# Kernel tuning notes

Hardware: AMD Instinct MI355X
Metric: run time of the kernel (lower is better)

## Reference

```python
import jax, jax.numpy as jnp
import numpy as np

N = 512          # octave output grid resolution per cube side
M = 256          # input octave resolution
FACTOR = 0.5     # 2 ** (-factor), factor = 1
EPS = 1e-12


def make_cube_faces(n):
    # two triangles per quad on each of the 6 n x n side grids
    idx = np.arange(n * n).reshape(n, n)
    a = idx[:-1, :-1].ravel(); b = idx[:-1, 1:].ravel()
    c = idx[1:, :-1].ravel(); d = idx[1:, 1:].ravel()
    tris = np.concatenate([np.stack([a, b, c], 1), np.stack([b, d, c], 1)], 0)
    faces = np.concatenate([tris + s * n * n for s in range(6)], 0)
    return jnp.asarray(faces, jnp.int32)  # [F, 3]


def to_stacked(t):
    # [1, 6*m*m, 3] -> [6, 3, m, m]
    m = int(round((t.shape[1] // 6) ** 0.5))
    return t.reshape(6, m, m, 3).transpose(0, 3, 1, 2)


def to_vertices(s):
    # [6, 3, m, m] -> [1, 6*m*m, 3]
    return s.transpose(0, 2, 3, 1).reshape(1, -1, 3)


def resize_bilinear_ac(t, n):
    # bilinear, align_corners=True, square input [.., m, m] -> [.., n, n]
    m = t.shape[-1]
    coords = jnp.linspace(0.0, m - 1.0, n)
    i0 = jnp.clip(jnp.floor(coords).astype(jnp.int32), 0, m - 1)
    i1 = jnp.minimum(i0 + 1, m - 1)
    w = (coords - i0).astype(t.dtype)
    t = t[..., i0, :] * (1.0 - w)[:, None] + t[..., i1, :] * w[:, None]
    t = t[..., :, i0] * (1.0 - w) + t[..., :, i1] * w
    return t


def compute_face_normals(vert, faces):
    v = vert[0]                                  # [V, 3]
    v0, v1, v2 = v[faces[:, 0]], v[faces[:, 1]], v[faces[:, 2]]
    fn = jnp.cross(v1 - v0, v2 - v0)             # [F, 3]
    nrm = jnp.linalg.norm(fn, axis=-1, keepdims=True)
    return fn / jnp.maximum(nrm, EPS)


def compute_vertex_normals(vert, faces, face_normals):
    V = vert.shape[1]
    flat_idx = faces.reshape(-1)                          # [3F] f0v0,f0v1,f0v2,...
    rep = jnp.repeat(face_normals, 3, axis=0)             # [3F, 3]
    acc = jax.ops.segment_sum(rep, flat_idx, num_segments=V)  # scatter-add
    nrm = jnp.linalg.norm(acc, axis=-1, keepdims=True)
    return (acc / jnp.maximum(nrm, EPS))[None]            # [1, V, 3]


def get_vertex_normals(vert, faces):
    fn = compute_face_normals(vert, faces)
    normals = compute_vertex_normals(vert, faces, fn)
    stacked = to_stacked(normals)                         # [6, 3, n, n]
    sign = jnp.array([-1.0, 1.0, 1.0, -1.0, -1.0, 1.0], stacked.dtype)
    stacked = stacked * sign[:, None, None, None]
    return to_vertices(stacked)


def setup_inputs() -> dict:
    key = jax.random.key(0)
    k1, k2 = jax.random.split(key)
    vrt = jax.random.normal(k1, (1, 6 * M * M, 3), jnp.float32)
    nrm = jax.random.normal(k2, (1, 6 * M * M, 3), jnp.float32)
    ps = jnp.zeros((6, 1, N, N), jnp.float32)   # nn.Parameter(zeros * noise)
    faces = make_cube_faces(N)
    return {"vrt": vrt, "nrm": nrm, "ps": ps, "faces": faces}


def reference(vrt, nrm, ps, faces):
    vrt_s = resize_bilinear_ac(to_stacked(vrt), N)                 # [6,3,n,n]
    nrm_mag = jnp.linalg.norm(resize_bilinear_ac(to_stacked(nrm), N),
                              axis=1, keepdims=True)               # [6,1,n,n]
    stacked = vrt_s + FACTOR * jax.nn.sigmoid(ps) * nrm_mag
    vert = to_vertices(stacked)                                    # [1, V, 3]
    normals = get_vertex_normals(vert, faces)
    return vert, faces, normals
```

## Files before the change

kernel.cpp:

```cpp
#include <hip/hip_runtime.h>
#include <math.h>

#define NSZ 512
#define MSZ 256
#define NPIX (6 * NSZ * NSZ)
#define NQ   ((NSZ - 1) * (NSZ - 1))
#define NFACE (6 * 2 * NQ)
#define F3TOT (NFACE * 3)
#define TS 32
#define HS (TS + 2)
#define PS 20
#define NVB (6 * 16 * 16)
#define NFT12 (F3TOT / 12)
#define GRID (NVB * 3)

__device__ inline float fast_rcp(float x) {
    float r = __builtin_amdgcn_rcpf(x);
    return r * (2.0f - x * r);
}
__device__ inline float fast_rsqrt(float d) {
    float r = __builtin_amdgcn_rsqf(d);
    return r * (1.5f - 0.5f * d * r * r);
}
__device__ inline float fast_sigmoid(float x) {
    float e = __builtin_amdgcn_exp2f(-1.442695040888963f * x);
    return fast_rcp(1.0f + e);
}

__device__ inline void tri_acc4(const float4 A, const float4 B, const float4 C,
                                float& ax, float& ay, float& az) {
    float e1x = B.x - A.x, e1y = B.y - A.y, e1z = B.z - A.z;
    float e2x = C.x - A.x, e2y = C.y - A.y, e2z = C.z - A.z;
    float nx = e1y * e2z - e1z * e2y;
    float ny = e1z * e2x - e1x * e2z;
    float nz = e1x * e2y - e1y * e2x;
    float d  = fmaxf(nx * nx + ny * ny + nz * nz, 1e-24f);
    float r  = fast_rsqrt(d);
    ax += nx * r; ay += ny * r; az += nz * r;
}

__global__ __launch_bounds__(256) void k_all(const float* __restrict__ vrt,
                                             const float* __restrict__ nrm,
                                             const float* __restrict__ ps,
                                             float* __restrict__ out0,
                                             float* __restrict__ out1,
                                             float* __restrict__ out2) {
    __shared__ float4 spv[PS * PS];
    __shared__ float4 spn[PS * PS];
    __shared__ float4 sv4[HS * HS];

    int blk    = blockIdx.x;
    int triple = blk / 3;
    int pos    = blk - triple * 3;

    if (pos != 0) {
        int t = (triple * 2 + (pos - 1)) * 256 + threadIdx.x;
        if (t >= NFT12) return;
        unsigned ti = 4u * (unsigned)t;
        unsigned s  = ti / (2u * NQ);
        unsigned r1 = ti - s * (2u * NQ);
        unsigned ty = (r1 >= (unsigned)NQ) ? 1u : 0u;
        unsigned qi = r1 - ty * (unsigned)NQ;
        unsigned R  = qi / (NSZ - 1);
        unsigned Q  = qi - R * (NSZ - 1);
        unsigned sbase = s << 18;
        float v[12];
#pragma unroll
        for (int k = 0; k < 4; ++k) {
            unsigned a = sbase + (R << 9) + Q;
            v[3 * k + 0] = (float)(a + (ty ? 1u : 0u));
            v[3 * k + 1] = (float)(a + (ty ? (unsigned)(NSZ + 1) : 1u));
            v[3 * k + 2] = (float)(a + (unsigned)NSZ);
            Q++;
            if (Q == (unsigned)(NSZ - 1)) {
                Q = 0u; R++;
                if (R == (unsigned)(NSZ - 1)) {
                    R = 0u; ty++;
                    if (ty == 2u) { ty = 0u; sbase += (unsigned)(NSZ * NSZ); }
                }
            }
        }
        float4* o = (float4*)out1 + 3 * t;
        o[0] = make_float4(v[0], v[1], v[2],  v[3]);
        o[1] = make_float4(v[4], v[5], v[6],  v[7]);
        o[2] = make_float4(v[8], v[9], v[10], v[11]);
        return;
    }

    int f   = triple >> 8;
    int tl  = triple & 255;
    int tr  = (tl >> 4) * TS;
    int tq  = (tl & 15) * TS;
    int fbm = f * (MSZ * MSZ);
    int fbn = f * (NSZ * NSZ);

    int iy_base = max(0, ((tr - 1) * (MSZ - 1)) / (NSZ - 1));
    int ix_base = max(0, ((tq - 1) * (MSZ - 1)) / (NSZ - 1));

    for (int p = threadIdx.x; p < PS * PS; p += 256) {
        int r = p / PS, c = p - r * PS;
        int iy = min(iy_base + r, MSZ - 1);
        int ix = min(ix_base + c, MSZ - 1);
        int g  = (fbm + iy * MSZ + ix) * 3;
        spv[p] = make_float4(vrt[g], vrt[g + 1], vrt[g + 2], 0.0f);
        spn[p] = make_float4(nrm[g], nrm[g + 1], nrm[g + 2], 0.0f);
    }
    __syncthreads();

    const float scale = 255.0f / 511.0f;
    for (int p = threadIdx.x; p < HS * HS; p += 256) {
        int pr = p / HS, pq = p - pr * HS;
        int y = tr + pr - 1, x = tq + pq - 1;
        int yc = min(max(y, 0), NSZ - 1);
        int xc = min(max(x, 0), NSZ - 1);

        float cy = (float)yc * scale;
        float cx = (float)xc * scale;
        int iy0 = (int)floorf(cy); iy0 = iy0 < 0 ? 0 : (iy0 > MSZ - 1 ? MSZ - 1 : iy0);
        int ix0 = (int)floorf(cx); ix0 = ix0 < 0 ? 0 : (ix0 > MSZ - 1 ? MSZ - 1 : ix0);
        int iy1 = min(iy0 + 1, MSZ - 1);
        int ix1 = min(ix0 + 1, MSZ - 1);
        float wy = cy - (float)iy0;
        float wx = cx - (float)ix0;
        float w00 = (1.0f - wy) * (1.0f - wx);
        float w01 = (1.0f - wy) * wx;
        float w10 = wy * (1.0f - wx);
        float w11 = wy * wx;

        int l00 = (iy0 - iy_base) * PS + (ix0 - ix_base);
        int l01 = (iy0 - iy_base) * PS + (ix1 - ix_base);
        int l10 = (iy1 - iy_base) * PS + (ix0 - ix_base);
        int l11 = (iy1 - iy_base) * PS + (ix1 - ix_base);

        float4 a00 = spv[l00], a01 = spv[l01], a10 = spv[l10], a11 = spv[l11];
        float4 b00 = spn[l00], b01 = spn[l01], b10 = spn[l10], b11 = spn[l11];

        float vx = a00.x * w00 + a01.x * w01 + a10.x * w10 + a11.x * w11;
        float vy = a00.y * w00 + a01.y * w01 + a10.y * w10 + a11.y * w11;
        float vz = a00.z * w00 + a01.z * w01 + a10.z * w10 + a11.z * w11;
        float nx = b00.x * w00 + b01.x * w01 + b10.x * w10 + b11.x * w11;
        float ny = b00.y * w00 + b01.y * w01 + b10.y * w10 + b11.y * w11;
        float nz = b00.z * w00 + b01.z * w01 + b10.z * w10 + b11.z * w11;

        float mag = __builtin_amdgcn_sqrtf(nx * nx + ny * ny + nz * nz);
        float sig = fast_sigmoid(ps[fbn + yc * NSZ + xc]);
        float add = 0.5f * sig * mag;
        float ox = vx + add, oy = vy + add, oz = vz + add;

        sv4[p] = make_float4(ox, oy, oz, 0.0f);
        if (pr >= 1 && pr <= TS && pq >= 1 && pq <= TS) {
            int gi = (fbn + y * NSZ + x) * 3;
            out0[gi + 0] = ox;
            out0[gi + 1] = oy;
            out0[gi + 2] = oz;
        }
    }
    __syncthreads();

    float sg = (f == 1 || f == 2 || f == 5) ? 1.0f : -1.0f;
    for (int p = threadIdx.x; p < TS * TS; p += 256) {
        int r = p >> 5, q = p & 31;
        int lc = (r + 1) * HS + (q + 1);
        float4 C  = sv4[lc];
        float4 W  = sv4[lc - 1];
        float4 E  = sv4[lc + 1];
        float4 Nn = sv4[lc - HS];
        float4 S  = sv4[lc + HS];
        float4 NE = sv4[lc - HS + 1];
        float4 SW = sv4[lc + HS - 1];

        float ax = 0.0f, ay = 0.0f, az = 0.0f;
        tri_acc4(C,  E,  S,  ax, ay, az);
        tri_acc4(W,  C,  SW, ax, ay, az);
        tri_acc4(Nn, NE, C,  ax, ay, az);
        tri_acc4(C,  S,  SW, ax, ay, az);
        tri_acc4(Nn, C,  W,  ax, ay, az);
        tri_acc4(NE, E,  C,  ax, ay, az);

        float d  = fmaxf(ax * ax + ay * ay + az * az, 1e-24f);
        float rs = fast_rsqrt(d) * sg;
        int gi = (fbn + (tr + r) * NSZ + (tq + q)) * 3;
        out2[gi + 0] = ax * rs;
        out2[gi + 1] = ay * rs;
        out2[gi + 2] = az * rs;
    }
}

extern "C" void kernel_launch(void* const* d_in, const int* in_sizes, int n_in,
                              void* d_out, int out_size, void* d_ws, size_t ws_size,
                              hipStream_t stream) {
    const float* vrt = (const float*)d_in[0];
    const float* nrm = (const float*)d_in[1];
    const float* ps  = (const float*)d_in[2];

    float* out0 = (float*)d_out;
    float* out1 = out0 + (size_t)NPIX * 3;
    float* out2 = out1 + (size_t)NFACE * 3;

    k_all<<<GRID, 256, 0, stream>>>(vrt, nrm, ps, out0, out1, out2);
}
```

Before: 32.27 us.

## Compute each triangle normal once per tile in shared memory, then gather per vertex

Replaces the per-vertex recomputation of six adjacent triangle normals with a separate pass that computes the two triangle normals per quad once into shared memory, masking quads that fall outside the mesh. A second pass sums the six incident normals per vertex. The tile is also stored as packed float triples instead of float4, and the shared-memory staging buffers are aliased. This removes about threefold redundant cross products and rsqrt calls, at the cost of an extra barrier pass and strided 3-float LDS accesses that may cause bank conflicts.

```diff
diff --git a/kernel.cpp b/kernel.cpp
--- a/kernel.cpp
+++ b/kernel.cpp
@@ -9,10 +9,12 @@
 #define F3TOT (NFACE * 3)
 #define TS 32
 #define HS (TS + 2)
+#define QS (TS + 1)
 #define PS 20
 #define NVB (6 * 16 * 16)
 #define NFT12 (F3TOT / 12)
 #define GRID (NVB * 3)
+#define USZ (2 * QS * QS * 3)
 
 __device__ inline float fast_rcp(float x) {
     float r = __builtin_amdgcn_rcpf(x);
@@ -25,18 +27,6 @@
 __device__ inline float fast_sigmoid(float x) {
     float e = __builtin_amdgcn_exp2f(-1.442695040888963f * x);
     return fast_rcp(1.0f + e);
-}
-
-__device__ inline void tri_acc4(const float4 A, const float4 B, const float4 C,
-                                float& ax, float& ay, float& az) {
-    float e1x = B.x - A.x, e1y = B.y - A.y, e1z = B.z - A.z;
-    float e2x = C.x - A.x, e2y = C.y - A.y, e2z = C.z - A.z;
-    float nx = e1y * e2z - e1z * e2y;
-    float ny = e1z * e2x - e1x * e2z;
-    float nz = e1x * e2y - e1y * e2x;
-    float d  = fmaxf(nx * nx + ny * ny + nz * nz, 1e-24f);
-    float r  = fast_rsqrt(d);
-    ax += nx * r; ay += ny * r; az += nz * r;
 }
 
 __global__ __launch_bounds__(256) void k_all(const float* __restrict__ vrt,
@@ -45,9 +35,12 @@
                                              float* __restrict__ out0,
                                              float* __restrict__ out1,
                                              float* __restrict__ out2) {
-    __shared__ float4 spv[PS * PS];
-    __shared__ float4 spn[PS * PS];
-    __shared__ float4 sv4[HS * HS];
+    __shared__ float sv[HS * HS * 3];
+    __shared__ __align__(16) float smem[USZ];
+    float4* spv = (float4*)smem;
+    float4* spn = ((float4*)smem) + PS * PS;
+    float*  tn0 = smem;
+    float*  tn1 = smem + QS * QS * 3;
 
     int blk    = blockIdx.x;
     int triple = blk / 3;
@@ -147,7 +140,9 @@
         float add = 0.5f * sig * mag;
         float ox = vx + add, oy = vy + add, oz = vz + add;
 
-        sv4[p] = make_float4(ox, oy, oz, 0.0f);
+        sv[p * 3 + 0] = ox;
+        sv[p * 3 + 1] = oy;
+        sv[p * 3 + 2] = oz;
         if (pr >= 1 && pr <= TS && pq >= 1 && pq <= TS) {
             int gi = (fbn + y * NSZ + x) * 3;
             out0[gi + 0] = ox;
@@ -157,25 +152,59 @@
     }
     __syncthreads();
 
+    for (int p = threadIdx.x; p < QS * QS; p += 256) {
+        int Ri = p / QS, Qi = p - Ri * QS;
+        bool valid = ((unsigned)(tr + Ri - 1) < (unsigned)(NSZ - 1)) &&
+                     ((unsigned)(tq + Qi - 1) < (unsigned)(NSZ - 1));
+        float msk = valid ? 1.0f : 0.0f;
+        #define SVL(rr, qq, c) sv[(((rr) * HS) + (qq)) * 3 + (c)]
+        float ax0 = SVL(Ri,   Qi,   0), ay0 = SVL(Ri,   Qi,   1), az0 = SVL(Ri,   Qi,   2);
+        float bx  = SVL(Ri,   Qi+1, 0), by  = SVL(Ri,   Qi+1, 1), bz  = SVL(Ri,   Qi+1, 2);
+        float cx  = SVL(Ri+1, Qi,   0), cy  = SVL(Ri+1, Qi,   1), cz  = SVL(Ri+1, Qi,   2);
+        float dx  = SVL(Ri+1, Qi+1, 0), dy  = SVL(Ri+1, Qi+1, 1), dz  = SVL(Ri+1, Qi+1, 2);
+        #undef SVL
+
+        {
+            float e1x = bx - ax0, e1y = by - ay0, e1z = bz - az0;
+            float e2x = cx - ax0, e2y = cy - ay0, e2z = cz - az0;
+            float nx = e1y * e2z - e1z * e2y;
+            float ny = e1z * e2x - e1x * e2z;
+            float nz = e1x * e2y - e1y * e2x;
+            float d  = fmaxf(nx * nx + ny * ny + nz * nz, 1e-24f);
+            float r  = fast_rsqrt(d) * msk;
+            tn0[p * 3 + 0] = nx * r;
+            tn0[p * 3 + 1] = ny * r;
+            tn0[p * 3 + 2] = nz * r;
+        }
+        {
+            float e1x = dx - bx, e1y = dy - by, e1z = dz - bz;
+            float e2x = cx - bx, e2y = cy - by, e2z = cz - bz;
+            float nx = e1y * e2z - e1z * e2y;
+            float ny = e1z * e2x - e1x * e2z;
+            float nz = e1x * e2y - e1y * e2x;
+            float d  = fmaxf(nx * nx + ny * ny + nz * nz, 1e-24f);
+            float r  = fast_rsqrt(d) * msk;
+            tn1[p * 3 + 0] = nx * r;
+            tn1[p * 3 + 1] = ny * r;
+            tn1[p * 3 + 2] = nz * r;
+        }
+    }
+    __syncthreads();
+
     float sg = (f == 1 || f == 2 || f == 5) ? 1.0f : -1.0f;
     for (int p = threadIdx.x; p < TS * TS; p += 256) {
         int r = p >> 5, q = p & 31;
-        int lc = (r + 1) * HS + (q + 1);
-        float4 C  = sv4[lc];
-        float4 W  = sv4[lc - 1];
-        float4 E  = sv4[lc + 1];
-        float4 Nn = sv4[lc - HS];
-        float4 S  = sv4[lc + HS];
-        float4 NE = sv4[lc - HS + 1];
-        float4 SW = sv4[lc + HS - 1];
-
-        float ax = 0.0f, ay = 0.0f, az = 0.0f;
-        tri_acc4(C,  E,  S,  ax, ay, az);
-        tri_acc4(W,  C,  SW, ax, ay, az);
-        tri_acc4(Nn, NE, C,  ax, ay, az);
-        tri_acc4(C,  S,  SW, ax, ay, az);
-        tri_acc4(Nn, C,  W,  ax, ay, az);
-        tri_acc4(NE, E,  C,  ax, ay, az);
+        int q00 = ((r    ) * QS + (q    )) * 3;
+        int q01 = ((r    ) * QS + (q + 1)) * 3;
+        int q10 = ((r + 1) * QS + (q    )) * 3;
+        int q11 = ((r + 1) * QS + (q + 1)) * 3;
+
+        float ax = tn0[q11 + 0] + tn0[q10 + 0] + tn0[q01 + 0]
+                 + tn1[q10 + 0] + tn1[q00 + 0] + tn1[q01 + 0];
+        float ay = tn0[q11 + 1] + tn0[q10 + 1] + tn0[q01 + 1]
+                 + tn1[q10 + 1] + tn1[q00 + 1] + tn1[q01 + 1];
+        float az = tn0[q11 + 2] + tn0[q10 + 2] + tn0[q01 + 2]
+                 + tn1[q10 + 2] + tn1[q00 + 2] + tn1[q01 + 2];
 
         float d  = fmaxf(ax * ax + ay * ay + az * az, 1e-24f);
         float rs = fast_rsqrt(d) * sg;
```

New measurement: 30.94 us. 1.04x faster.
